# Kernel optimization log

Hardware: AMD Instinct MI355X
Metric: run time of the kernel (lower is better)

## Reference

```python
import jax, jax.numpy as jnp
import numpy as np

B, T, C = 8, 2048, 2048   # batch, seq, embedding
A = 2048                  # attn_dim
H, N = 32, 64             # heads, head_size
LORA_MIX, LORA_DEC = 32, 64
EPS = 1e-5 * 8 ** 2       # GroupNorm eps with head_size_divisor=8


def setup_inputs() -> dict:
    key = jax.random.key(0)
    ks = jax.random.split(key, 24)
    s = lambda k, shape, scale=1.0: jax.random.normal(k, shape, jnp.float32) * scale
    inp = {
        'x': s(ks[0], (B, T, C)),
        'time_maa_x': jax.random.uniform(ks[1], (1, 1, C)),
        'time_maa_w': jax.random.uniform(ks[2], (1, 1, C)),
        'time_maa_k': jax.random.uniform(ks[3], (1, 1, C)),
        'time_maa_v': jax.random.uniform(ks[4], (1, 1, C)),
        'time_maa_r': jax.random.uniform(ks[5], (1, 1, C)),
        'time_maa_g': jax.random.uniform(ks[6], (1, 1, C)),
        'maa_w1': s(ks[7], (C, LORA_MIX * 5), 0.01),
        'maa_w2': s(ks[8], (5, LORA_MIX, C), 0.01),
        'time_decay': s(ks[9], (1, 1, A)) - 4.0,   # decay_speed init is in [-6,-1]
        'decay_w1': s(ks[10], (C, LORA_DEC), 0.01),
        'decay_w2': s(ks[11], (LORA_DEC, A), 0.01),
        'u': s(ks[12], (H, N), 0.1),
        'Wr': s(ks[13], (A, C), C ** -0.5),
        'Wk': s(ks[14], (A, C), C ** -0.5),
        'Wv': s(ks[15], (A, C), C ** -0.5),
        'Wg': s(ks[16], (A, C), C ** -0.5),
        'Wo': s(ks[17], (C, A), A ** -0.5),
        'ln_w': jnp.ones((A,), jnp.float32),
        'ln_b': jnp.zeros((A,), jnp.float32),
    }
    return inp


def wkv6(r, k, v, dec, u):
    # r,k,v,dec: (B,T,A) -> (T,B,H,N); dec already exp(-exp(w))
    def to_tbhn(a):
        return a.reshape(B, T, H, N).transpose(1, 0, 2, 3)
    rr, kk, vv, dd = map(to_tbhn, (r, k, v, dec))

    def step(S, inp):  # S: (B,H,N,N) indexed [key_chan i, val_chan j]
        rt, kt, vt, dt = inp
        a = kt[..., :, None] * vt[..., None, :]            # rank-1 update (B,H,N,N)
        y = jnp.einsum('bhi,bhij->bhj', rt, S + u[None, :, :, None] * a)
        S = dt[..., None] * S + a                          # per-key-channel decay
        return S, y

    S0 = jnp.zeros((B, H, N, N), r.dtype)
    _, y = jax.lax.scan(step, S0, (rr, kk, vv, dd))
    return y.transpose(1, 0, 2, 3).reshape(B, T, A)


def reference(x, time_maa_x, time_maa_w, time_maa_k, time_maa_v, time_maa_r,
              time_maa_g, maa_w1, maa_w2, time_decay, decay_w1, decay_w2,
              u, Wr, Wk, Wv, Wg, Wo, ln_w, ln_b):
    # token shift: x[t-1] - x[t] (zero-padded at t=0)
    xx = jnp.pad(x, ((0, 0), (1, 0), (0, 0)))[:, :T] - x
    xxx = x + xx * time_maa_x
    m = jnp.tanh(xxx @ maa_w1).reshape(B, T, 5, LORA_MIX)
    m = jnp.einsum('btfd,fdc->fbtc', m, maa_w2)            # (5,B,T,C)
    mw, mk, mv, mr, mg = m

    xw = x + xx * (time_maa_w + mw)
    xk = x + xx * (time_maa_k + mk)
    xv = x + xx * (time_maa_v + mv)
    xr = x + xx * (time_maa_r + mr)
    xg = x + xx * (time_maa_g + mg)

    r = xr @ Wr.T
    k = xk @ Wk.T
    v = xv @ Wv.T
    g = jax.nn.silu(xg @ Wg.T)
    w = time_decay + jnp.tanh(xw @ decay_w1) @ decay_w2
    dec = jnp.exp(-jnp.exp(w))                              # RWKV6 decay mapping

    y = wkv6(r, k, v, dec, u)

    # GroupNorm over each head's N channels
    yg = y.reshape(B, T, H, N)
    mu = yg.mean(-1, keepdims=True)
    var = yg.var(-1, keepdims=True)
    yn = ((yg - mu) * jax.lax.rsqrt(var + EPS)).reshape(B, T, A)
    yn = yn * ln_w + ln_b

    return (yn * g) @ Wo.T
```

## Files before the change

### kernel.cpp

```cpp
#include <hip/hip_runtime.h>
#include <hip/hip_bf16.h>
#include <cstdint>
#include <cstddef>

#define B_ 8
#define T_ 2048
#define C_ 2048
#define A_ 2048
#define H_ 32
#define BT_ (B_*T_)

typedef short short8 __attribute__((ext_vector_type(8)));
typedef _Float16 half8 __attribute__((ext_vector_type(8)));
typedef float floatx4 __attribute__((ext_vector_type(4)));

__device__ __forceinline__ unsigned short f2bf(float f) {
  union { float f; uint32_t u; } a; a.f = f;
  uint32_t r = a.u + 0x7fffu + ((a.u >> 16) & 1u);
  return (unsigned short)(r >> 16);
}
__device__ __forceinline__ float bf2f(unsigned short s) {
  union { uint32_t u; float f; } a; a.u = ((uint32_t)s) << 16;
  return a.f;
}
__device__ __forceinline__ unsigned short f2h(float f) {
  union { _Float16 h; unsigned short u; } c; c.h = (_Float16)f; return c.u;
}
__device__ __forceinline__ float h2f(unsigned short u) {
  union { unsigned short u; _Float16 h; } c; c.u = u; return (float)c.h;
}
__device__ __forceinline__ void split_hl(float v, unsigned short& hh, unsigned short& ll) {
  hh = f2bf(v);
  ll = f2bf(v - bf2f(hh));
}
__device__ __forceinline__ int swz(int row, int col) {
  return row * 64 + (col ^ ((row & 7) << 3));
}
__device__ __forceinline__ short8 ldfrag(const unsigned short* M, int row, int col8) {
  return *(const short8*)&M[row * 64 + (col8 ^ ((row & 7) << 3))];
}

__global__ void conv_f16(const float* __restrict__ s, unsigned short* __restrict__ d, int n) {
  int i = blockIdx.x * 256 + threadIdx.x;
  if (i < n) d[i] = f2h(s[i]);
}

__global__ void transpose_pad(const float* __restrict__ s, unsigned short* __restrict__ d, int NP, int NV) {
  int i = blockIdx.x * 256 + threadIdx.x;
  int n = i >> 11, kk = i & 2047;
  if (n < NP) d[i] = (n < NV) ? f2h(s[kk * NV + n]) : (unsigned short)0;
}

__global__ void transpose_w2(const float* __restrict__ s, unsigned short* __restrict__ d) {
  int i = blockIdx.x * 256 + threadIdx.x;
  int f = i >> 16, rem = i & 65535;
  int dd = rem >> 11, c = rem & 2047;
  d[((size_t)(f * 2048 + c) << 5) + dd] = f2h(s[((size_t)(f * 32 + dd) << 11) + c]);
}

__global__ void shift_mix(const float* __restrict__ x, const float* __restrict__ tmx,
                          unsigned short* __restrict__ xxx) {
  size_t i4 = (size_t)blockIdx.x * 256 + threadIdx.x;
  size_t i = i4 * 4;
  int c = (int)(i & 2047);
  int t = (int)((i >> 11) & 2047);
  float4 xv = *(const float4*)&x[i];
  float4 pv = make_float4(0.f, 0.f, 0.f, 0.f);
  if (t > 0) pv = *(const float4*)&x[i - 2048];
  float4 tv = *(const float4*)&tmx[c];
  ushort4 m;
  m.x = f2h(xv.x + (pv.x - xv.x) * tv.x);
  m.y = f2h(xv.y + (pv.y - xv.y) * tv.y);
  m.z = f2h(xv.z + (pv.z - xv.z) * tv.z);
  m.w = f2h(xv.w + (pv.w - xv.w) * tv.w);
  *(ushort4*)&xxx[i] = m;
}

__device__ __forceinline__ void gll16(const void* g, void* l) {
  __builtin_amdgcn_global_load_lds(
      (const __attribute__((address_space(1))) void*)g,
      (__attribute__((address_space(3))) void*)l, 16, 0, 0);
}

template<int EPI>
__global__ __launch_bounds__(256)
void gemm_f16(const unsigned short* __restrict__ Am, const unsigned short* __restrict__ Bm,
              void* __restrict__ Cp, int M, int N, int K) {
  __shared__ unsigned short As[128 * 32];
  __shared__ unsigned short Bs[128 * 32];
  const int tid = threadIdx.x;
  const int wid = tid >> 6, lane = tid & 63;
  const int quad = lane >> 4, l15 = lane & 15;
  const long bm = (long)blockIdx.x * 128, bn = (long)blockIdx.y * 128;
  const int wm = (wid & 1) * 64, wn = (wid >> 1) * 64;

  floatx4 acc[4][4];
#pragma unroll
  for (int a = 0; a < 4; a++)
#pragma unroll
    for (int b = 0; b < 4; b++) { floatx4 z = {0.f, 0.f, 0.f, 0.f}; acc[a][b] = z; }

  const int stg_row = wid * 32 + (lane >> 2);
  const int stg_k   = (lane & 3) * 8;
  const int stg_lds = wid * 1024 + lane * 8;

  for (int k0 = 0; k0 < K; k0 += 32) {
    __syncthreads();
#pragma unroll
    for (int p = 0; p < 2; ++p) {
      gll16(Am + (bm + stg_row + p * 16) * (long)K + k0 + stg_k, &As[stg_lds + p * 512]);
      gll16(Bm + (bn + stg_row + p * 16) * (long)K + k0 + stg_k, &Bs[stg_lds + p * 512]);
    }
    __syncthreads();

    half8 af[4], bfr[4];
#pragma unroll
    for (int mi = 0; mi < 4; mi++) af[mi] = *(const half8*)&As[(wm + mi * 16 + l15) * 32 + quad * 8];
#pragma unroll
    for (int ni = 0; ni < 4; ni++) bfr[ni] = *(const half8*)&Bs[(wn + ni * 16 + l15) * 32 + quad * 8];
#pragma unroll
    for (int mi = 0; mi < 4; mi++)
#pragma unroll
      for (int ni = 0; ni < 4; ni++)
        acc[mi][ni] = __builtin_amdgcn_mfma_f32_16x16x32_f16(af[mi], bfr[ni], acc[mi][ni], 0, 0, 0);
  }

#pragma unroll
  for (int mi = 0; mi < 4; mi++)
#pragma unroll
    for (int ni = 0; ni < 4; ni++)
#pragma unroll
      for (int vv = 0; vv < 4; ++vv) {
        long row = bm + wm + mi * 16 + quad * 4 + vv;
        long col = bn + wn + ni * 16 + l15;
        float val = acc[mi][ni][vv];
        if (EPI == 0) {
          ((unsigned short*)Cp)[row * N + col] = f2bf(val);
        } else if (EPI == 1) {
          float s = val / (1.f + __expf(-val));
          ((unsigned short*)Cp)[row * N + col] = f2h(s);
        } else if (EPI == 2) {
          ((float*)Cp)[row * N + col] = tanhf(val);
        } else if (EPI == 4) {
          ((unsigned short*)Cp)[row * N + col] = f2h(tanhf(val));
        } else {
          ((float*)Cp)[row * N + col] = val;
        }
      }
}

template<int EPI>
__global__ __launch_bounds__(512, 2)
void gemm256(const unsigned short* __restrict__ Am, const unsigned short* __restrict__ Bm,
             void* __restrict__ Cp, int M, int N, int K) {
  __shared__ unsigned short At[4][8192];
  __shared__ unsigned short Bt[4][8192];
  const int tid = threadIdx.x;
  const int w = tid >> 6, lane = tid & 63;
  const int quad = lane >> 4, l15 = lane & 15;
  const long bm = (long)blockIdx.x * 256, bn = (long)blockIdx.y * 256;
  const int wm = (w & 1) * 128, wn = (w >> 1) * 64;

  floatx4 acc[8][4];
#pragma unroll
  for (int a = 0; a < 8; a++)
#pragma unroll
    for (int b = 0; b < 4; b++) { floatx4 z = {0.f, 0.f, 0.f, 0.f}; acc[a][b] = z; }

  int srow[2], scol[2];
#pragma unroll
  for (int u = 0; u < 2; ++u) {
    int p = u * 8192 + tid * 16;
    int l = p ^ (((p >> 6) & 3) << 4);
    srow[u] = l >> 6;
    scol[u] = (l & 63) >> 1;
  }
  const int ldst = tid * 16;

  const int NT = K >> 5;
  for (int t = 0; t < 3; ++t) {
#pragma unroll
    for (int u = 0; u < 2; ++u) {
      gll16(Am + (bm + srow[u]) * (long)K + (t << 5) + scol[u],
            (char*)&At[t][0] + u * 8192 + ldst);
      gll16(Bm + (bn + srow[u]) * (long)K + (t << 5) + scol[u],
            (char*)&Bt[t][0] + u * 8192 + ldst);
    }
  }
  asm volatile("s_waitcnt vmcnt(8) lgkmcnt(0)\n\ts_barrier" ::: "memory");

  for (int t = 0; t < NT; ++t) {
    const int bi = t & 3;
    const unsigned short* Ab = At[bi];
    const unsigned short* Bb = Bt[bi];
    const int tn = t + 3;
    const bool do_stage = tn < NT;
    const int bj = tn & 3;

    if (do_stage) {
      gll16(Am + (bm + srow[0]) * (long)K + (tn << 5) + scol[0], (char*)&At[bj][0] + ldst);
      gll16(Bm + (bn + srow[0]) * (long)K + (tn << 5) + scol[0], (char*)&Bt[bj][0] + ldst);
    }
    half8 bfr[4], af[4];
#pragma unroll
    for (int ni = 0; ni < 4; ++ni) {
      int r = wn + ni * 16 + l15;
      bfr[ni] = *(const half8*)((const char*)Bb + r * 64 + ((quad ^ (r & 3)) << 4));
    }
#pragma unroll
    for (int mi = 0; mi < 4; ++mi) {
      int r = wm + mi * 16 + l15;
      af[mi] = *(const half8*)((const char*)Ab + r * 64 + ((quad ^ (r & 3)) << 4));
    }
    __builtin_amdgcn_s_setprio(1);
#pragma unroll
    for (int mi = 0; mi < 4; ++mi)
#pragma unroll
      for (int ni = 0; ni < 4; ++ni)
        acc[mi][ni] = __builtin_amdgcn_mfma_f32_16x16x32_f16(af[mi], bfr[ni], acc[mi][ni], 0, 0, 0);
    __builtin_amdgcn_s_setprio(0);

    if (do_stage) {
      gll16(Am + (bm + srow[1]) * (long)K + (tn << 5) + scol[1], (char*)&At[bj][0] + 8192 + ldst);
      gll16(Bm + (bn + srow[1]) * (long)K + (tn << 5) + scol[1], (char*)&Bt[bj][0] + 8192 + ldst);
    }
#pragma unroll
    for (int mi = 0; mi < 4; ++mi) {
      int r = wm + 64 + mi * 16 + l15;
      af[mi] = *(const half8*)((const char*)Ab + r * 64 + ((quad ^ (r & 3)) << 4));
    }
    __builtin_amdgcn_s_setprio(1);
#pragma unroll
    for (int mi = 0; mi < 4; ++mi)
#pragma unroll
      for (int ni = 0; ni < 4; ++ni)
        acc[4 + mi][ni] = __builtin_amdgcn_mfma_f32_16x16x32_f16(af[mi], bfr[ni], acc[4 + mi][ni], 0, 0, 0);
    __builtin_amdgcn_s_setprio(0);

    asm volatile("s_waitcnt vmcnt(8) lgkmcnt(0)\n\ts_barrier" ::: "memory");
  }

#pragma unroll
  for (int p = 0; p < 2; ++p)
#pragma unroll
    for (int mi = 0; mi < 4; ++mi)
#pragma unroll
      for (int ni = 0; ni < 4; ++ni)
#pragma unroll
        for (int vv = 0; vv < 4; ++vv) {
          long row = bm + wm + p * 64 + mi * 16 + quad * 4 + vv;
          long col = bn + wn + ni * 16 + l15;
          float val = acc[p * 4 + mi][ni][vv];
          if (EPI == 0) {
            ((unsigned short*)Cp)[row * N + col] = f2bf(val);
          } else if (EPI == 1) {
            float s = val / (1.f + __expf(-val));
            ((unsigned short*)Cp)[row * N + col] = f2h(s);
          } else {
            ((float*)Cp)[row * N + col] = val;
          }
        }
}

__global__ __launch_bounds__(256)
void mix_gemm(const unsigned short* __restrict__ m5f, const unsigned short* __restrict__ w2T,
              const float* __restrict__ x,
              const float* __restrict__ tmw, const float* __restrict__ tmk,
              const float* __restrict__ tmv, const float* __restrict__ tmr,
              const float* __restrict__ tmg,
              unsigned short* __restrict__ xw, unsigned short* __restrict__ xk,
              unsigned short* __restrict__ xv, unsigned short* __restrict__ xr,
              unsigned short* __restrict__ xg) {
  __shared__ unsigned short As[128 * 32];
  __shared__ unsigned short Bs[128 * 32];
  const int tid = threadIdx.x;
  const int wid = tid >> 6, lane = tid & 63;
  const int quad = lane >> 4, l15 = lane & 15;
  const long bm = (long)blockIdx.x * 128, bn = (long)blockIdx.y * 128;
  const int f = blockIdx.z;
  const int wm = (wid & 1) * 64, wn = (wid >> 1) * 64;

  const float* tmf = (f == 0) ? tmw : (f == 1) ? tmk : (f == 2) ? tmv : (f == 3) ? tmr : tmg;
  unsigned short* outf = (f == 0) ? xw : (f == 1) ? xk : (f == 2) ? xv : (f == 3) ? xr : xg;

  const int stg_row = wid * 32 + (lane >> 2);
  const int stg_k   = (lane & 3) * 8;
  const int stg_lds = wid * 1024 + lane * 8;

#pragma unroll
  for (int p = 0; p < 2; ++p) {
    gll16(m5f + (bm + stg_row + p * 16) * 256 + f * 32 + stg_k, &As[stg_lds + p * 512]);
    gll16(w2T + ((long)f * 2048 + bn + stg_row + p * 16) * 32 + stg_k, &Bs[stg_lds + p * 512]);
  }
  __syncthreads();

  half8 af[4], bfr[4];
#pragma unroll
  for (int mi = 0; mi < 4; mi++) af[mi] = *(const half8*)&As[(wm + mi * 16 + l15) * 32 + quad * 8];
#pragma unroll
  for (int ni = 0; ni < 4; ni++) bfr[ni] = *(const half8*)&Bs[(wn + ni * 16 + l15) * 32 + quad * 8];

  floatx4 acc[4][4];
#pragma unroll
  for (int a = 0; a < 4; a++)
#pragma unroll
    for (int b = 0; b < 4; b++) { floatx4 z = {0.f, 0.f, 0.f, 0.f}; acc[a][b] = z; }
#pragma unroll
  for (int mi = 0; mi < 4; mi++)
#pragma unroll
    for (int ni = 0; ni < 4; ni++)
      acc[mi][ni] = __builtin_amdgcn_mfma_f32_16x16x32_f16(af[mi], bfr[ni], acc[mi][ni], 0, 0, 0);

#pragma unroll
  for (int ni = 0; ni < 4; ni++) {
    const long col = bn + wn + ni * 16 + l15;
    const float tv = tmf[col];
#pragma unroll
    for (int mi = 0; mi < 4; mi++) {
      const long row0 = bm + wm + mi * 16 + quad * 4;
      const size_t idx0 = (size_t)row0 * 2048 + col;
      float xc[4];
#pragma unroll
      for (int vv = 0; vv < 4; ++vv) xc[vv] = x[idx0 + (size_t)vv * 2048];
      float xprev = ((row0 & 2047) > 0) ? x[idx0 - 2048] : 0.f;
#pragma unroll
      for (int vv = 0; vv < 4; ++vv) {
        const float xp = vv ? xc[vv - 1] : xprev;
        outf[idx0 + (size_t)vv * 2048] = f2h(xc[vv] + (xp - xc[vv]) * (tv + acc[mi][ni][vv]));
      }
    }
  }
}

__global__ __launch_bounds__(256)
void decay_kernel(const float* __restrict__ t1, const float* __restrict__ w2d,
                  const float* __restrict__ td, float* __restrict__ dec) {
  const int bt0 = blockIdx.x * 16;
  const int tid = threadIdx.x;
  for (int cc = 0; cc < 8; ++cc) {
    const int a = cc * 256 + tid;
    const float tda = td[a];
    float acc[16];
#pragma unroll
    for (int b = 0; b < 16; b++) acc[b] = 0.f;
    for (int dc = 0; dc < 16; ++dc) {
      float wv0 = w2d[((size_t)(dc * 4 + 0) << 11) + a];
      float wv1 = w2d[((size_t)(dc * 4 + 1) << 11) + a];
      float wv2 = w2d[((size_t)(dc * 4 + 2) << 11) + a];
      float wv3 = w2d[((size_t)(dc * 4 + 3) << 11) + a];
#pragma unroll
      for (int b = 0; b < 16; b++) {
        float4 mv = *(const float4*)&t1[((size_t)(bt0 + b) << 7) + dc * 4];
        acc[b] += mv.x * wv0 + mv.y * wv1 + mv.z * wv2 + mv.w * wv3;
      }
    }
#pragma unroll
    for (int b = 0; b < 16; b++) {
      dec[((size_t)(bt0 + b) << 11) + a] = __expf(-__expf(tda + acc[b]));
    }
  }
}

template<int KF32>
__global__ __launch_bounds__(512, 1)
void wkv6_chunk(const unsigned short* __restrict__ r, const unsigned short* __restrict__ k16,
                const float* __restrict__ k32, const float* __restrict__ v,
                const float* __restrict__ dec, const float* __restrict__ u,
                unsigned short* __restrict__ gz,
                const float* __restrict__ lnw, const float* __restrict__ lnb) {
  __shared__ unsigned short Rh[4096], Rl[4096];
  __shared__ unsigned short Kh[4096], Kl[4096];
  __shared__ unsigned short KTh[4096], KTl[4096];
  __shared__ unsigned short VTh[4096], VTl[4096];
  __shared__ unsigned short Amh[4096], Aml[4096];
  __shared__ unsigned short SThi[4096], STlo[4096];
  __shared__ float STf[4096];
  __shared__ float qpart[8][64];
  __shared__ float LcEnd[64];
  __shared__ float diagv[64];
  __shared__ float gnp[8][16][2];

  const int bh = blockIdx.x, b = bh >> 5, h = bh & 31;
  const int tid = threadIdx.x;
  const int w = tid >> 6, lane = tid & 63;
  const int quad = lane >> 4, l15 = lane & 15;
  const int cb = h * 64;
  const int wr = w >> 1, wc = w & 1;
  const int rq = w * 8;
  const int mrow = wr * 16;
  const int mcol = wc * 32;

  const float uu = u[cb + lane];
  float lnwv[2], lnbv[2];
#pragma unroll
  for (int ni = 0; ni < 2; ++ni) {
    lnwv[ni] = lnw[cb + mcol + ni * 16 + l15];
    lnbv[ni] = lnb[cb + mcol + ni * 16 + l15];
  }

  for (int i = tid; i < 4096; i += 512) STf[i] = 0.f;

  const size_t bT = (size_t)b * T_;

  float dA[8], rA[8], kA[8], vA[8];
  {
    const size_t ro = (bT + rq) * (size_t)A_ + cb + lane;
#pragma unroll
    for (int q = 0; q < 8; ++q) {
      const size_t o = ro + (size_t)q * A_;
      dA[q] = dec[o];
      rA[q] = bf2f(r[o]);
      if (KF32) kA[q] = k32[o];
      else      kA[q] = bf2f(k16[o]);
      vA[q] = v[o];
    }
  }

  for (int c = 0; c < T_ / 64; ++c) {
    const int t0 = c * 64;
    float lcq[8];
    lcq[0] = dA[0];
#pragma unroll
    for (int q = 1; q < 8; ++q) lcq[q] = lcq[q - 1] * dA[q];
    qpart[w][lane] = lcq[7];
    __syncthreads();
    {
      float pre = 1.f;
#pragma unroll
      for (int pw = 0; pw < 7; ++pw)
        if (pw < w) pre *= qpart[pw][lane];
      if (w == 7) LcEnd[lane] = pre * lcq[7];
      unsigned short hh, ll;
#pragma unroll
      for (int q = 0; q < 8; ++q) {
        const int jr = rq + q;
        split_hl(STf[jr * 64 + lane], hh, ll);
        const int ixs = swz(jr, lane);
        SThi[ixs] = hh; STlo[ixs] = ll;
      }
      short8 ktph, ktpl, vtph, vtpl;
#pragma unroll
      for (int q = 0; q < 8; ++q) {
        const int tr = rq + q;
        const float Pl = q ? pre * lcq[q - 1] : pre;
        const float Lc = pre * lcq[q];
        const int ix = swz(tr, lane);
        split_hl(rA[q] * Pl, hh, ll);
        Rh[ix] = hh; Rl[ix] = ll;
        const float kn = kA[q] / Lc;
        split_hl(kn, hh, ll);
        Kh[ix] = hh; Kl[ix] = ll;
        ktph[q] = (short)hh; ktpl[q] = (short)ll;
        split_hl(vA[q], hh, ll);
        vtph[q] = (short)hh; vtpl[q] = (short)ll;
        float dp = rA[q] * uu * kA[q];
        dp += __shfl_xor(dp, 1, 64);
        dp += __shfl_xor(dp, 2, 64);
        dp += __shfl_xor(dp, 4, 64);
        dp += __shfl_xor(dp, 8, 64);
        dp += __shfl_xor(dp, 16, 64);
        dp += __shfl_xor(dp, 32, 64);
        if (lane == 0) diagv[tr] = dp;
      }
      const int ixT = lane * 64 + (rq ^ ((lane & 7) << 3));
      *(short8*)&KTh[ixT] = ktph;
      *(short8*)&KTl[ixT] = ktpl;
      *(short8*)&VTh[ixT] = vtph;
      *(short8*)&VTl[ixT] = vtpl;
    }
    __syncthreads();
    if (c + 1 < T_ / 64) {
      const size_t ro = (bT + t0 + 64 + rq) * (size_t)A_ + cb + lane;
#pragma unroll
      for (int q = 0; q < 8; ++q) {
        const size_t o = ro + (size_t)q * A_;
        dA[q] = dec[o];
        rA[q] = bf2f(r[o]);
        if (KF32) kA[q] = k32[o];
        else      kA[q] = bf2f(k16[o]);
        vA[q] = v[o];
      }
    }
    {
      short8 arh[2], arl[2];
#pragma unroll
      for (int kst = 0; kst < 2; ++kst) {
        const int c8 = kst * 32 + quad * 8;
        arh[kst] = ldfrag(Rh, mrow + l15, c8);
        arl[kst] = ldfrag(Rl, mrow + l15, c8);
      }
      floatx4 acc[2];
#pragma unroll
      for (int ni = 0; ni < 2; ++ni) { floatx4 z = {0.f, 0.f, 0.f, 0.f}; acc[ni] = z; }
#pragma unroll
      for (int ni = 0; ni < 2; ++ni)
#pragma unroll
        for (int kst = 0; kst < 2; ++kst) {
          const int c8 = kst * 32 + quad * 8;
          short8 bh_ = ldfrag(Kh, mcol + ni * 16 + l15, c8);
          short8 bl_ = ldfrag(Kl, mcol + ni * 16 + l15, c8);
          acc[ni] = __builtin_amdgcn_mfma_f32_16x16x32_bf16(arh[kst], bh_, acc[ni], 0, 0, 0);
          acc[ni] = __builtin_amdgcn_mfma_f32_16x16x32_bf16(arh[kst], bl_, acc[ni], 0, 0, 0);
          acc[ni] = __builtin_amdgcn_mfma_f32_16x16x32_bf16(arl[kst], bh_, acc[ni], 0, 0, 0);
        }
#pragma unroll
      for (int ni = 0; ni < 2; ++ni)
#pragma unroll
        for (int vv = 0; vv < 4; ++vv) {
          const int grow = mrow + quad * 4 + vv;
          const int gcol = mcol + ni * 16 + l15;
          float val = (grow > gcol) ? acc[ni][vv] : ((grow == gcol) ? diagv[grow] : 0.f);
          unsigned short hh, ll;
          split_hl(val, hh, ll);
          const int ix = swz(grow, gcol);
          Amh[ix] = hh; Aml[ix] = ll;
        }
    }
    __syncthreads();
    {
      short8 aAh[2], aAl[2], aRh[2], aRl[2];
#pragma unroll
      for (int kst = 0; kst < 2; ++kst) {
        const int c8 = kst * 32 + quad * 8;
        aAh[kst] = ldfrag(Amh, mrow + l15, c8);
        aAl[kst] = ldfrag(Aml, mrow + l15, c8);
        aRh[kst] = ldfrag(Rh, mrow + l15, c8);
        aRl[kst] = ldfrag(Rl, mrow + l15, c8);
      }
      floatx4 acc[2];
#pragma unroll
      for (int ni = 0; ni < 2; ++ni) { floatx4 z = {0.f, 0.f, 0.f, 0.f}; acc[ni] = z; }
#pragma unroll
      for (int ni = 0; ni < 2; ++ni)
#pragma unroll
        for (int kst = 0; kst < 2; ++kst) {
          const int c8 = kst * 32 + quad * 8;
          const int brow = mcol + ni * 16 + l15;
          short8 bvh = ldfrag(VTh, brow, c8);
          short8 bvl = ldfrag(VTl, brow, c8);
          acc[ni] = __builtin_amdgcn_mfma_f32_16x16x32_bf16(aAh[kst], bvh, acc[ni], 0, 0, 0);
          acc[ni] = __builtin_amdgcn_mfma_f32_16x16x32_bf16(aAh[kst], bvl, acc[ni], 0, 0, 0);
          acc[ni] = __builtin_amdgcn_mfma_f32_16x16x32_bf16(aAl[kst], bvh, acc[ni], 0, 0, 0);
          short8 bsh = ldfrag(SThi, brow, c8);
          short8 bsl = ldfrag(STlo, brow, c8);
          acc[ni] = __builtin_amdgcn_mfma_f32_16x16x32_bf16(aRh[kst], bsh, acc[ni], 0, 0, 0);
          acc[ni] = __builtin_amdgcn_mfma_f32_16x16x32_bf16(aRh[kst], bsl, acc[ni], 0, 0, 0);
          acc[ni] = __builtin_amdgcn_mfma_f32_16x16x32_bf16(aRl[kst], bsh, acc[ni], 0, 0, 0);
        }
      float s1_[4], s2_[4];
#pragma unroll
      for (int vv = 0; vv < 4; ++vv) {
        float s1 = acc[0][vv] + acc[1][vv];
        float s2 = acc[0][vv] * acc[0][vv] + acc[1][vv] * acc[1][vv];
        s1 += __shfl_xor(s1, 1, 64); s2 += __shfl_xor(s2, 1, 64);
        s1 += __shfl_xor(s1, 2, 64); s2 += __shfl_xor(s2, 2, 64);
        s1 += __shfl_xor(s1, 4, 64); s2 += __shfl_xor(s2, 4, 64);
        s1 += __shfl_xor(s1, 8, 64); s2 += __shfl_xor(s2, 8, 64);
        s1_[vv] = s1; s2_[vv] = s2;
        if (l15 == 0) {
          gnp[w][quad * 4 + vv][0] = s1;
          gnp[w][quad * 4 + vv][1] = s2;
        }
      }
      __syncthreads();
#pragma unroll
      for (int ni = 0; ni < 2; ++ni)
#pragma unroll
        for (int vv = 0; vv < 4; ++vv) {
          const int rloc = quad * 4 + vv;
          float s1 = s1_[vv] + gnp[w ^ 1][rloc][0];
          float s2 = s2_[vv] + gnp[w ^ 1][rloc][1];
          float mu = s1 * (1.f / 64.f);
          float var = s2 * (1.f / 64.f) - mu * mu;
          float rs = rsqrtf(var + 6.4e-4f);
          const size_t off = (bT + t0 + mrow + rloc) * (size_t)A_ + cb + mcol + ni * 16 + l15;
          float yn = (acc[ni][vv] - mu) * rs * lnwv[ni] + lnbv[ni];
          float z = yn * h2f(gz[off]);
          gz[off] = f2h(z);
        }
    }
    {
      short8 avh[2], avl[2];
#pragma unroll
      for (int kst = 0; kst < 2; ++kst) {
        const int c8 = kst * 32 + quad * 8;
        avh[kst] = ldfrag(VTh, mrow + l15, c8);
        avl[kst] = ldfrag(VTl, mrow + l15, c8);
      }
      floatx4 a4[2];
#pragma unroll
      for (int ni = 0; ni < 2; ++ni) { floatx4 z = {0.f, 0.f, 0.f, 0.f}; a4[ni] = z; }
#pragma unroll
      for (int ni = 0; ni < 2; ++ni)
#pragma unroll
        for (int kst = 0; kst < 2; ++kst) {
          const int c8 = kst * 32 + quad * 8;
          short8 bkh = ldfrag(KTh, mcol + ni * 16 + l15, c8);
          short8 bkl = ldfrag(KTl, mcol + ni * 16 + l15, c8);
          a4[ni] = __builtin_amdgcn_mfma_f32_16x16x32_bf16(avh[kst], bkh, a4[ni], 0, 0, 0);
          a4[ni] = __builtin_amdgcn_mfma_f32_16x16x32_bf16(avh[kst], bkl, a4[ni], 0, 0, 0);
          a4[ni] = __builtin_amdgcn_mfma_f32_16x16x32_bf16(avl[kst], bkh, a4[ni], 0, 0, 0);
        }
#pragma unroll
      for (int ni = 0; ni < 2; ++ni) {
        const float lce = LcEnd[mcol + ni * 16 + l15];
#pragma unroll
        for (int vv = 0; vv < 4; ++vv) {
          const int jr = mrow + quad * 4 + vv;
          const int ic = mcol + ni * 16 + l15;
          STf[jr * 64 + ic] = lce * (a4[ni][vv] + STf[jr * 64 + ic]);
        }
      }
    }
    __syncthreads();
  }
}

extern "C" void kernel_launch(void* const* d_in, const int* in_sizes, int n_in,
                              void* d_out, int out_size, void* d_ws, size_t ws_size,
                              hipStream_t stream) {
  (void)in_sizes; (void)n_in; (void)out_size;
  const float* x   = (const float*)d_in[0];
  const float* tmx = (const float*)d_in[1];
  const float* tmw = (const float*)d_in[2];
  const float* tmk = (const float*)d_in[3];
  const float* tmv = (const float*)d_in[4];
  const float* tmr = (const float*)d_in[5];
  const float* tmg = (const float*)d_in[6];
  const float* w1  = (const float*)d_in[7];
  const float* w2  = (const float*)d_in[8];
  const float* td  = (const float*)d_in[9];
  const float* dw1 = (const float*)d_in[10];
  const float* dw2 = (const float*)d_in[11];
  const float* u   = (const float*)d_in[12];
  const float* Wr  = (const float*)d_in[13];
  const float* Wk  = (const float*)d_in[14];
  const float* Wv  = (const float*)d_in[15];
  const float* Wg  = (const float*)d_in[16];
  const float* Wo  = (const float*)d_in[17];
  const float* lnw = (const float*)d_in[18];
  const float* lnb = (const float*)d_in[19];

  char* ws = (char*)d_ws;
  const size_t MB = 1024 * 1024;
  unsigned short* xxx  = (unsigned short*)(ws + 0 * MB);
  unsigned short* gb   = (unsigned short*)(ws + 0 * MB);
  unsigned short* m5   = (unsigned short*)(ws + 64 * MB);
  float*          vf   = (float*)(ws + 64 * MB);
  unsigned short* w1T  = (unsigned short*)(ws + 128 * MB);
  unsigned short* bxk  = (unsigned short*)(ws + 128 * MB);
  unsigned short* bxv  = (unsigned short*)(ws + 192 * MB);
  float*          decb = (float*)(ws + 192 * MB);
  unsigned short* bxw  = (unsigned short*)(ws + 256 * MB);
  unsigned short* bxg  = (unsigned short*)(ws + 320 * MB);
  unsigned short* rb   = (unsigned short*)(ws + 320 * MB);
  unsigned short* bxr  = (unsigned short*)(ws + 384 * MB);
  unsigned short* kb   = (unsigned short*)(ws + 384 * MB);
  unsigned short* dw1T = (unsigned short*)(ws + 448 * MB);
  unsigned short* Wf   = (unsigned short*)(ws + 448 * MB);
  unsigned short* w2T  = (unsigned short*)(ws + 460 * MB);
  float*          t1   = (float*)(ws + 464 * MB);
  const bool kf32 = ws_size >= (size_t)616 * MB;
  float* kf = (float*)(ws + 480 * MB);

  const int nW = A_ * C_;
  const size_t EBT = (size_t)BT_ * C_;

  shift_mix<<<(int)(EBT / 4 / 256), 256, 0, stream>>>(x, tmx, xxx);

  transpose_pad<<<(256 * 2048) / 256, 256, 0, stream>>>(w1, w1T, 256, 160);
  gemm_f16<4><<<dim3(BT_ / 128, 2), 256, 0, stream>>>(xxx, w1T, m5, BT_, 256, 2048);

  transpose_w2<<<(5 * 65536) / 256, 256, 0, stream>>>(w2, w2T);
  mix_gemm<<<dim3(BT_ / 128, C_ / 128, 5), 256, 0, stream>>>(m5, w2T, x,
                                                             tmw, tmk, tmv, tmr, tmg,
                                                             bxw, bxk, bxv, bxr, bxg);

  transpose_pad<<<(128 * 2048) / 256, 256, 0, stream>>>(dw1, dw1T, 128, 64);
  gemm_f16<2><<<dim3(BT_ / 128, 1), 256, 0, stream>>>(bxw, dw1T, t1, BT_, 128, 2048);

  conv_f16<<<nW / 256, 256, 0, stream>>>(Wg, Wf, nW);
  gemm256<1><<<dim3(BT_ / 256, C_ / 256), 512, 0, stream>>>(bxg, Wf, gb, BT_, 2048, 2048);
  conv_f16<<<nW / 256, 256, 0, stream>>>(Wr, Wf, nW);
  gemm256<0><<<dim3(BT_ / 256, C_ / 256), 512, 0, stream>>>(bxr, Wf, rb, BT_, 2048, 2048);
  conv_f16<<<nW / 256, 256, 0, stream>>>(Wk, Wf, nW);
  if (kf32) {
    gemm256<3><<<dim3(BT_ / 256, C_ / 256), 512, 0, stream>>>(bxk, Wf, kf, BT_, 2048, 2048);
  } else {
    gemm256<0><<<dim3(BT_ / 256, C_ / 256), 512, 0, stream>>>(bxk, Wf, kb, BT_, 2048, 2048);
  }
  conv_f16<<<nW / 256, 256, 0, stream>>>(Wv, Wf, nW);
  gemm256<3><<<dim3(BT_ / 256, C_ / 256), 512, 0, stream>>>(bxv, Wf, vf, BT_, 2048, 2048);

  decay_kernel<<<BT_ / 16, 256, 0, stream>>>(t1, dw2, td, decb);

  if (kf32) {
    wkv6_chunk<1><<<256, 512, 0, stream>>>(rb, kb, kf, vf, decb, u, gb, lnw, lnb);
  } else {
    wkv6_chunk<0><<<256, 512, 0, stream>>>(rb, kb, kf, vf, decb, u, gb, lnw, lnb);
  }

  conv_f16<<<nW / 256, 256, 0, stream>>>(Wo, Wf, nW);
  gemm256<3><<<dim3(BT_ / 256, C_ / 256), 512, 0, stream>>>(gb, Wf, (float*)d_out, BT_, 2048, 2048);
}
```

Before: 2.013 ms.

## Double wkv6 chunk block to 16 waves and keep state in split bf16

The chunked WKV6 kernel now runs 1024 threads (16 waves) per (batch, head) block instead of 512. Each wave owns one 16x16 output tile and four timesteps rather than two tiles and eight. The fp32 state array in shared memory is removed; the state is kept only as hi/lo bf16 pairs and updated in place. The decay-prefix computation moves to the end of the previous iteration, which removes one barrier per chunk. This aims to add parallelism on only 256 blocks and cut per-chunk latency. The costs are extra rounding from storing the state as bf16 pairs and more cross-wave reduction for the group norm.

Result: slower. 2.109 ms (+4.7%).

```diff
diff --git a/kernel.cpp b/kernel.cpp
--- a/kernel.cpp
+++ b/kernel.cpp
@@ -362,7 +362,7 @@
 }
 
 template<int KF32>
-__global__ __launch_bounds__(512, 1)
+__global__ __launch_bounds__(1024, 1)
 void wkv6_chunk(const unsigned short* __restrict__ r, const unsigned short* __restrict__ k16,
                 const float* __restrict__ k32, const float* __restrict__ v,
                 const float* __restrict__ dec, const float* __restrict__ u,
@@ -374,39 +374,34 @@
   __shared__ unsigned short VTh[4096], VTl[4096];
   __shared__ unsigned short Amh[4096], Aml[4096];
   __shared__ unsigned short SThi[4096], STlo[4096];
-  __shared__ float STf[4096];
-  __shared__ float qpart[8][64];
+  __shared__ float qpart[16][64];
   __shared__ float LcEnd[64];
   __shared__ float diagv[64];
-  __shared__ float gnp[8][16][2];
+  __shared__ float gnp[16][16][2];
 
   const int bh = blockIdx.x, b = bh >> 5, h = bh & 31;
   const int tid = threadIdx.x;
   const int w = tid >> 6, lane = tid & 63;
   const int quad = lane >> 4, l15 = lane & 15;
   const int cb = h * 64;
-  const int wr = w >> 1, wc = w & 1;
-  const int rq = w * 8;
+  const int wr = w >> 2, wc = w & 3;
+  const int rq = w * 4;
   const int mrow = wr * 16;
-  const int mcol = wc * 32;
+  const int mcol = wc * 16;
 
   const float uu = u[cb + lane];
-  float lnwv[2], lnbv[2];
-#pragma unroll
-  for (int ni = 0; ni < 2; ++ni) {
-    lnwv[ni] = lnw[cb + mcol + ni * 16 + l15];
-    lnbv[ni] = lnb[cb + mcol + ni * 16 + l15];
-  }
-
-  for (int i = tid; i < 4096; i += 512) STf[i] = 0.f;
+  const float lnwv = lnw[cb + mcol + l15];
+  const float lnbv = lnb[cb + mcol + l15];
+
+  for (int i = tid; i < 4096; i += 1024) { SThi[i] = 0; STlo[i] = 0; }
 
   const size_t bT = (size_t)b * T_;
 
-  float dA[8], rA[8], kA[8], vA[8];
+  float dA[4], rA[4], kA[4], vA[4], lcq[4];
   {
     const size_t ro = (bT + rq) * (size_t)A_ + cb + lane;
 #pragma unroll
-    for (int q = 0; q < 8; ++q) {
+    for (int q = 0; q < 4; ++q) {
       const size_t o = ro + (size_t)q * A_;
       dA[q] = dec[o];
       rA[q] = bf2f(r[o]);
@@ -415,32 +410,24 @@
       vA[q] = v[o];
     }
   }
+  lcq[0] = dA[0];
+#pragma unroll
+  for (int q = 1; q < 4; ++q) lcq[q] = lcq[q - 1] * dA[q];
+  qpart[w][lane] = lcq[3];
+  __syncthreads();
 
   for (int c = 0; c < T_ / 64; ++c) {
     const int t0 = c * 64;
-    float lcq[8];
-    lcq[0] = dA[0];
-#pragma unroll
-    for (int q = 1; q < 8; ++q) lcq[q] = lcq[q - 1] * dA[q];
-    qpart[w][lane] = lcq[7];
-    __syncthreads();
     {
       float pre = 1.f;
 #pragma unroll
-      for (int pw = 0; pw < 7; ++pw)
+      for (int pw = 0; pw < 15; ++pw)
         if (pw < w) pre *= qpart[pw][lane];
-      if (w == 7) LcEnd[lane] = pre * lcq[7];
+      if (w == 15) LcEnd[lane] = pre * lcq[3];
       unsigned short hh, ll;
-#pragma unroll
-      for (int q = 0; q < 8; ++q) {
-        const int jr = rq + q;
-        split_hl(STf[jr * 64 + lane], hh, ll);
-        const int ixs = swz(jr, lane);
-        SThi[ixs] = hh; STlo[ixs] = ll;
-      }
-      short8 ktph, ktpl, vtph, vtpl;
-#pragma unroll
-      for (int q = 0; q < 8; ++q) {
+      ushort4 ktph, ktpl, vtph, vtpl;
+#pragma unroll
+      for (int q = 0; q < 4; ++q) {
         const int tr = rq + q;
         const float Pl = q ? pre * lcq[q - 1] : pre;
         const float Lc = pre * lcq[q];
@@ -450,9 +437,9 @@
         const float kn = kA[q] / Lc;
         split_hl(kn, hh, ll);
         Kh[ix] = hh; Kl[ix] = ll;
-        ktph[q] = (short)hh; ktpl[q] = (short)ll;
+        ((unsigned short*)&ktph)[q] = hh; ((unsigned short*)&ktpl)[q] = ll;
         split_hl(vA[q], hh, ll);
-        vtph[q] = (short)hh; vtpl[q] = (short)ll;
+        ((unsigned short*)&vtph)[q] = hh; ((unsigned short*)&vtpl)[q] = ll;
         float dp = rA[q] * uu * kA[q];
         dp += __shfl_xor(dp, 1, 64);
         dp += __shfl_xor(dp, 2, 64);
@@ -463,16 +450,16 @@
         if (lane == 0) diagv[tr] = dp;
       }
       const int ixT = lane * 64 + (rq ^ ((lane & 7) << 3));
-      *(short8*)&KTh[ixT] = ktph;
-      *(short8*)&KTl[ixT] = ktpl;
-      *(short8*)&VTh[ixT] = vtph;
-      *(short8*)&VTl[ixT] = vtpl;
+      *(ushort4*)&KTh[ixT] = ktph;
+      *(ushort4*)&KTl[ixT] = ktpl;
+      *(ushort4*)&VTh[ixT] = vtph;
+      *(ushort4*)&VTl[ixT] = vtpl;
     }
     __syncthreads();
     if (c + 1 < T_ / 64) {
       const size_t ro = (bT + t0 + 64 + rq) * (size_t)A_ + cb + lane;
 #pragma unroll
-      for (int q = 0; q < 8; ++q) {
+      for (int q = 0; q < 4; ++q) {
         const size_t o = ro + (size_t)q * A_;
         dA[q] = dec[o];
         rA[q] = bf2f(r[o]);
@@ -482,76 +469,56 @@
       }
     }
     {
-      short8 arh[2], arl[2];
+      floatx4 acc = {0.f, 0.f, 0.f, 0.f};
 #pragma unroll
       for (int kst = 0; kst < 2; ++kst) {
         const int c8 = kst * 32 + quad * 8;
-        arh[kst] = ldfrag(Rh, mrow + l15, c8);
-        arl[kst] = ldfrag(Rl, mrow + l15, c8);
-      }
-      floatx4 acc[2];
-#pragma unroll
-      for (int ni = 0; ni < 2; ++ni) { floatx4 z = {0.f, 0.f, 0.f, 0.f}; acc[ni] = z; }
-#pragma unroll
-      for (int ni = 0; ni < 2; ++ni)
-#pragma unroll
-        for (int kst = 0; kst < 2; ++kst) {
-          const int c8 = kst * 32 + quad * 8;
-          short8 bh_ = ldfrag(Kh, mcol + ni * 16 + l15, c8);
-          short8 bl_ = ldfrag(Kl, mcol + ni * 16 + l15, c8);
-          acc[ni] = __builtin_amdgcn_mfma_f32_16x16x32_bf16(arh[kst], bh_, acc[ni], 0, 0, 0);
-          acc[ni] = __builtin_amdgcn_mfma_f32_16x16x32_bf16(arh[kst], bl_, acc[ni], 0, 0, 0);
-          acc[ni] = __builtin_amdgcn_mfma_f32_16x16x32_bf16(arl[kst], bh_, acc[ni], 0, 0, 0);
-        }
-#pragma unroll
-      for (int ni = 0; ni < 2; ++ni)
-#pragma unroll
-        for (int vv = 0; vv < 4; ++vv) {
-          const int grow = mrow + quad * 4 + vv;
-          const int gcol = mcol + ni * 16 + l15;
-          float val = (grow > gcol) ? acc[ni][vv] : ((grow == gcol) ? diagv[grow] : 0.f);
-          unsigned short hh, ll;
-          split_hl(val, hh, ll);
-          const int ix = swz(grow, gcol);
-          Amh[ix] = hh; Aml[ix] = ll;
-        }
+        short8 arh = ldfrag(Rh, mrow + l15, c8);
+        short8 arl = ldfrag(Rl, mrow + l15, c8);
+        short8 bh_ = ldfrag(Kh, mcol + l15, c8);
+        short8 bl_ = ldfrag(Kl, mcol + l15, c8);
+        acc = __builtin_amdgcn_mfma_f32_16x16x32_bf16(arh, bh_, acc, 0, 0, 0);
+        acc = __builtin_amdgcn_mfma_f32_16x16x32_bf16(arh, bl_, acc, 0, 0, 0);
+        acc = __builtin_amdgcn_mfma_f32_16x16x32_bf16(arl, bh_, acc, 0, 0, 0);
+      }
+#pragma unroll
+      for (int vv = 0; vv < 4; ++vv) {
+        const int grow = mrow + quad * 4 + vv;
+        const int gcol = mcol + l15;
+        float val = (grow > gcol) ? acc[vv] : ((grow == gcol) ? diagv[grow] : 0.f);
+        unsigned short hh, ll;
+        split_hl(val, hh, ll);
+        const int ix = swz(grow, gcol);
+        Amh[ix] = hh; Aml[ix] = ll;
+      }
     }
     __syncthreads();
+    floatx4 acc3 = {0.f, 0.f, 0.f, 0.f};
+    float s1_[4], s2_[4];
     {
-      short8 aAh[2], aAl[2], aRh[2], aRl[2];
 #pragma unroll
       for (int kst = 0; kst < 2; ++kst) {
         const int c8 = kst * 32 + quad * 8;
-        aAh[kst] = ldfrag(Amh, mrow + l15, c8);
-        aAl[kst] = ldfrag(Aml, mrow + l15, c8);
-        aRh[kst] = ldfrag(Rh, mrow + l15, c8);
-        aRl[kst] = ldfrag(Rl, mrow + l15, c8);
-      }
-      floatx4 acc[2];
-#pragma unroll
-      for (int ni = 0; ni < 2; ++ni) { floatx4 z = {0.f, 0.f, 0.f, 0.f}; acc[ni] = z; }
-#pragma unroll
-      for (int ni = 0; ni < 2; ++ni)
-#pragma unroll
-        for (int kst = 0; kst < 2; ++kst) {
-          const int c8 = kst * 32 + quad * 8;
-          const int brow = mcol + ni * 16 + l15;
-          short8 bvh = ldfrag(VTh, brow, c8);
-          short8 bvl = ldfrag(VTl, brow, c8);
-          acc[ni] = __builtin_amdgcn_mfma_f32_16x16x32_bf16(aAh[kst], bvh, acc[ni], 0, 0, 0);
-          acc[ni] = __builtin_amdgcn_mfma_f32_16x16x32_bf16(aAh[kst], bvl, acc[ni], 0, 0, 0);
-          acc[ni] = __builtin_amdgcn_mfma_f32_16x16x32_bf16(aAl[kst], bvh, acc[ni], 0, 0, 0);
-          short8 bsh = ldfrag(SThi, brow, c8);
-          short8 bsl = ldfrag(STlo, brow, c8);
-          acc[ni] = __builtin_amdgcn_mfma_f32_16x16x32_bf16(aRh[kst], bsh, acc[ni], 0, 0, 0);
-          acc[ni] = __builtin_amdgcn_mfma_f32_16x16x32_bf16(aRh[kst], bsl, acc[ni], 0, 0, 0);
-          acc[ni] = __builtin_amdgcn_mfma_f32_16x16x32_bf16(aRl[kst], bsh, acc[ni], 0, 0, 0);
-        }
-      float s1_[4], s2_[4];
+        short8 aAh = ldfrag(Amh, mrow + l15, c8);
+        short8 aAl = ldfrag(Aml, mrow + l15, c8);
+        short8 aRh = ldfrag(Rh, mrow + l15, c8);
+        short8 aRl = ldfrag(Rl, mrow + l15, c8);
+        const int brow = mcol + l15;
+        short8 bvh = ldfrag(VTh, brow, c8);
+        short8 bvl = ldfrag(VTl, brow, c8);
+        acc3 = __builtin_amdgcn_mfma_f32_16x16x32_bf16(aAh, bvh, acc3, 0, 0, 0);
+        acc3 = __builtin_amdgcn_mfma_f32_16x16x32_bf16(aAh, bvl, acc3, 0, 0, 0);
+        acc3 = __builtin_amdgcn_mfma_f32_16x16x32_bf16(aAl, bvh, acc3, 0, 0, 0);
+        short8 bsh = ldfrag(SThi, brow, c8);
+        short8 bsl = ldfrag(STlo, brow, c8);
+        acc3 = __builtin_amdgcn_mfma_f32_16x16x32_bf16(aRh, bsh, acc3, 0, 0, 0);
+        acc3 = __builtin_amdgcn_mfma_f32_16x16x32_bf16(aRh, bsl, acc3, 0, 0, 0);
+        acc3 = __builtin_amdgcn_mfma_f32_16x16x32_bf16(aRl, bsh, acc3, 0, 0, 0);
+      }
 #pragma unroll
       for (int vv = 0; vv < 4; ++vv) {
-        float s1 = acc[0][vv] + acc[1][vv];
-        float s2 = acc[0][vv] * acc[0][vv] + acc[1][vv] * acc[1][vv];
+        float s1 = acc3[vv];
+        float s2 = acc3[vv] * acc3[vv];
         s1 += __shfl_xor(s1, 1, 64); s2 += __shfl_xor(s2, 1, 64);
         s1 += __shfl_xor(s1, 2, 64); s2 += __shfl_xor(s2, 2, 64);
         s1 += __shfl_xor(s1, 4, 64); s2 += __shfl_xor(s2, 4, 64);
@@ -562,55 +529,56 @@
           gnp[w][quad * 4 + vv][1] = s2;
         }
       }
-      __syncthreads();
-#pragma unroll
-      for (int ni = 0; ni < 2; ++ni)
-#pragma unroll
-        for (int vv = 0; vv < 4; ++vv) {
-          const int rloc = quad * 4 + vv;
-          float s1 = s1_[vv] + gnp[w ^ 1][rloc][0];
-          float s2 = s2_[vv] + gnp[w ^ 1][rloc][1];
-          float mu = s1 * (1.f / 64.f);
-          float var = s2 * (1.f / 64.f) - mu * mu;
-          float rs = rsqrtf(var + 6.4e-4f);
-          const size_t off = (bT + t0 + mrow + rloc) * (size_t)A_ + cb + mcol + ni * 16 + l15;
-          float yn = (acc[ni][vv] - mu) * rs * lnwv[ni] + lnbv[ni];
-          float z = yn * h2f(gz[off]);
-          gz[off] = f2h(z);
-        }
-    }
+    }
+    __syncthreads();
     {
-      short8 avh[2], avl[2];
+#pragma unroll
+      for (int vv = 0; vv < 4; ++vv) {
+        const int rloc = quad * 4 + vv;
+        float s1 = gnp[wr * 4 + 0][rloc][0] + gnp[wr * 4 + 1][rloc][0]
+                 + gnp[wr * 4 + 2][rloc][0] + gnp[wr * 4 + 3][rloc][0];
+        float s2 = gnp[wr * 4 + 0][rloc][1] + gnp[wr * 4 + 1][rloc][1]
+                 + gnp[wr * 4 + 2][rloc][1] + gnp[wr * 4 + 3][rloc][1];
+        float mu = s1 * (1.f / 64.f);
+        float var = s2 * (1.f / 64.f) - mu * mu;
+        float rs = rsqrtf(var + 6.4e-4f);
+        const size_t off = (bT + t0 + mrow + rloc) * (size_t)A_ + cb + mcol + l15;
+        float yn = (acc3[vv] - mu) * rs * lnwv + lnbv;
+        float z = yn * h2f(gz[off]);
+        gz[off] = f2h(z);
+      }
+    }
+    {
+      floatx4 a4 = {0.f, 0.f, 0.f, 0.f};
 #pragma unroll
       for (int kst = 0; kst < 2; ++kst) {
         const int c8 = kst * 32 + quad * 8;
-        avh[kst] = ldfrag(VTh, mrow + l15, c8);
-        avl[kst] = ldfrag(VTl, mrow + l15, c8);
-      }
-      floatx4 a4[2];
-#pragma unroll
-      for (int ni = 0; ni < 2; ++ni) { floatx4 z = {0.f, 0.f, 0.f, 0.f}; a4[ni] = z; }
-#pragma unroll
-      for (int ni = 0; ni < 2; ++ni)
-#pragma unroll
-        for (int kst = 0; kst < 2; ++kst) {
-          const int c8 = kst * 32 + quad * 8;
-          short8 bkh = ldfrag(KTh, mcol + ni * 16 + l15, c8);
-          short8 bkl = ldfrag(KTl, mcol + ni * 16 + l15, c8);
-          a4[ni] = __builtin_amdgcn_mfma_f32_16x16x32_bf16(avh[kst], bkh, a4[ni], 0, 0, 0);
-          a4[ni] = __builtin_amdgcn_mfma_f32_16x16x32_bf16(avh[kst], bkl, a4[ni], 0, 0, 0);
-          a4[ni] = __builtin_amdgcn_mfma_f32_16x16x32_bf16(avl[kst], bkh, a4[ni], 0, 0, 0);
-        }
-#pragma unroll
-      for (int ni = 0; ni < 2; ++ni) {
-        const float lce = LcEnd[mcol + ni * 16 + l15];
-#pragma unroll
-        for (int vv = 0; vv < 4; ++vv) {
-          const int jr = mrow + quad * 4 + vv;
-          const int ic = mcol + ni * 16 + l15;
-          STf[jr * 64 + ic] = lce * (a4[ni][vv] + STf[jr * 64 + ic]);
-        }
-      }
+        short8 avh = ldfrag(VTh, mrow + l15, c8);
+        short8 avl = ldfrag(VTl, mrow + l15, c8);
+        short8 bkh = ldfrag(KTh, mcol + l15, c8);
+        short8 bkl = ldfrag(KTl, mcol + l15, c8);
+        a4 = __builtin_amdgcn_mfma_f32_16x16x32_bf16(avh, bkh, a4, 0, 0, 0);
+        a4 = __builtin_amdgcn_mfma_f32_16x16x32_bf16(avh, bkl, a4, 0, 0, 0);
+        a4 = __builtin_amdgcn_mfma_f32_16x16x32_bf16(avl, bkh, a4, 0, 0, 0);
+      }
+      const float lce = LcEnd[mcol + l15];
+#pragma unroll
+      for (int vv = 0; vv < 4; ++vv) {
+        const int jr = mrow + quad * 4 + vv;
+        const int ic = mcol + l15;
+        const int ix = swz(jr, ic);
+        float sold = bf2f(SThi[ix]) + bf2f(STlo[ix]);
+        float snew = lce * (a4[vv] + sold);
+        unsigned short hh, ll;
+        split_hl(snew, hh, ll);
+        SThi[ix] = hh; STlo[ix] = ll;
+      }
+    }
+    if (c + 1 < T_ / 64) {
+      lcq[0] = dA[0];
+#pragma unroll
+      for (int q = 1; q < 4; ++q) lcq[q] = lcq[q - 1] * dA[q];
+      qpart[w][lane] = lcq[3];
     }
     __syncthreads();
   }
@@ -695,9 +663,9 @@
   decay_kernel<<<BT_ / 16, 256, 0, stream>>>(t1, dw2, td, decb);
 
   if (kf32) {
-    wkv6_chunk<1><<<256, 512, 0, stream>>>(rb, kb, kf, vf, decb, u, gb, lnw, lnb);
+    wkv6_chunk<1><<<256, 1024, 0, stream>>>(rb, kb, kf, vf, decb, u, gb, lnw, lnb);
   } else {
-    wkv6_chunk<0><<<256, 512, 0, stream>>>(rb, kb, kf, vf, decb, u, gb, lnw, lnb);
+    wkv6_chunk<0><<<256, 1024, 0, stream>>>(rb, kb, kf, vf, decb, u, gb, lnw, lnb);
   }
 
   conv_f16<<<nW / 256, 256, 0, stream>>>(Wo, Wf, nW);
```
